# Kernel tuning notes

Hardware: AMD Instinct MI355X
Metric: run time of the kernel (lower is better)

## Reference

```python
import jax, jax.numpy as jnp
import numpy as np

B, X, H, R, M = 256, 512, 1024, 512, 512
F_BIAS = 1.0

def setup_inputs() -> dict:
    key = jax.random.key(0)
    ks = jax.random.split(key, 8)
    s = lambda fan: 1.0 / np.sqrt(fan)
    return {
        "x": jax.random.normal(ks[0], (B, X), jnp.float32),
        "h": jax.random.normal(ks[1], (B, H), jnp.float32),
        "c": jnp.tanh(jax.random.normal(ks[2], (B, H), jnp.float32)),
        "hmem": jax.random.normal(ks[3], (B, M, R), jnp.float32),
        "W_full": jax.random.normal(ks[4], (X + R + H, R + 4 * H), jnp.float32) * s(X + R + H),
        "bias": jnp.zeros((R + 4 * H,), jnp.float32),
        "W_full1": jax.random.normal(ks[5], (X + R + H, R + H), jnp.float32) * s(X + R + H),
        "bias1": jnp.zeros((R + H,), jnp.float32),
        "trans_w": jax.random.normal(ks[6], (R, X + H), jnp.float32) * s(X + H),
        "trans_b": jnp.zeros((R,), jnp.float32),
        "fc_w": jax.random.normal(ks[7], (M, X + H), jnp.float32) * s(X + H),
        "fc_b": jnp.zeros((M,), jnp.float32),
    }

def reference(x, h, c, hmem, W_full, bias, W_full1, bias1, trans_w, trans_b, fc_w, fc_b):
    h_size = H
    # soft read head over memory slots
    read_head = jnp.concatenate([x, c], axis=1) @ fc_w.T + fc_b          # [B, M]
    h_index = jax.nn.softmax(read_head, axis=1)                          # [B, M]
    h_entry = jnp.einsum('bm,bmr->br', h_index, hmem)                    # [B, R]
    # gated double-projection
    concat = jnp.concatenate([x, c, h_entry], axis=1)                    # [B, X+H+R]
    g = jax.nn.sigmoid(concat @ W_full1 + bias1)                         # [B, R+H]
    gate = jnp.concatenate([jnp.ones_like(x), g], axis=1)                # [B, X+H+R]
    pre = (concat * gate) @ W_full + bias                                # [B, R+4H]
    i = pre[:, 0*h_size:1*h_size]
    j = pre[:, 1*h_size:2*h_size]
    f = pre[:, 2*h_size:3*h_size]
    o = pre[:, 3*h_size:4*h_size]
    om = pre[:, 4*h_size:]                                               # [B, R]
    new_c = jnp.tanh(c * jax.nn.sigmoid(f + F_BIAS) + jax.nn.sigmoid(i) * jnp.tanh(j))
    new_h = new_c * jax.nn.sigmoid(o)
    r_out = h_entry * jax.nn.sigmoid(om)
    # steady-state write: soft index (detached), broadcast overwrite
    w_index = jax.lax.stop_gradient(h_index)                             # [B, M]
    w_val = jnp.concatenate([x, new_c], axis=1) @ trans_w.T + trans_b    # [B, R]
    new_hmem = w_val[:, None, :] * w_index[:, :, None] + hmem * (1.0 - w_index[:, :, None])
    new_r = jnp.concatenate([new_h, r_out], axis=1)                      # [B, H+R]
    return new_r, new_h, new_c, new_hmem
```

## Files before the change

### kernel.cpp

```cpp
#include <hip/hip_runtime.h>
#include <hip/hip_bf16.h>
#include <cstddef>

#define BB 256
#define XX 512
#define HH 1024
#define RR 512
#define MM 512
#define KCAT 2048
#define KXC 1536
#define NFULL 4608
#define NG 1536

#define OFF_NH (BB*1536)
#define OFF_NC (OFF_NH + BB*HH)
#define OFF_HM (OFF_NC + BB*HH)

#define WS_HIDX   0
#define WS_CONCAT (WS_HIDX + BB*MM)
#define WS_GATED  (WS_CONCAT + BB*KCAT)
#define WS_PRE    (WS_GATED + BB*KCAT)
#define WS_WVAL   (WS_PRE + BB*NFULL)

typedef __attribute__((ext_vector_type(8))) short bf16x8;
typedef __attribute__((ext_vector_type(4))) short s16x4;
typedef __attribute__((ext_vector_type(4))) float f32x4;

__device__ __forceinline__ float sigm(float x) { return 1.0f / (1.0f + expf(-x)); }

__device__ __forceinline__ unsigned short f2bf(float f) {
    unsigned u = __float_as_uint(f);
    u = u + 0x7fffu + ((u >> 16) & 1u);
    return (unsigned short)(u >> 16);
}
__device__ __forceinline__ float bf2f(unsigned short h) {
    return __uint_as_float((unsigned)h << 16);
}

__global__ __launch_bounds__(256) void prep_k(const float* __restrict__ x,
                                              const float* __restrict__ c,
                                              float* __restrict__ concatb,
                                              float* __restrict__ gated) {
    int idx = blockIdx.x * 256 + threadIdx.x;
    int b = idx / KXC, q = idx - b * KXC;
    float v;
    if (q < XX) {
        v = x[b * XX + q];
        gated[(size_t)b * KCAT + q] = v;
    } else {
        v = c[b * HH + (q - XX)];
    }
    concatb[(size_t)b * KCAT + q] = v;
}

template<int AMODE, int BLAYOUT, int EPI>
__global__ __launch_bounds__(256) void mgemm_k(const float* __restrict__ A0,
                                               const float* __restrict__ A1,
                                               const float* __restrict__ W,
                                               const float* __restrict__ bias,
                                               float* __restrict__ C,
                                               const float* __restrict__ E,
                                               int N, int K) {
    __shared__ __align__(16) short Ah[64][72];
    __shared__ __align__(16) short Al[64][72];
    __shared__ __align__(16) short Bh[64][72];
    __shared__ __align__(16) short Bl[64][72];

    const int tid = threadIdx.x;
    const int row0 = blockIdx.y * 64, col0 = blockIdx.x * 64;
    const int lane = tid & 63, w = tid >> 6;
    const int rm = (w >> 1) * 32, cn = (w & 1) * 32;
    const int fr = lane & 15;
    const int kg = lane >> 4;

    const int ar = tid >> 2;
    const int akq = (tid & 3) * 16;
    const int bkk = (tid >> 4) * 4;
    const int bnn = (tid & 15) * 4;

    f32x4 acc[2][2] = {};

    for (int k0 = 0; k0 < K; k0 += 64) {
        {
            const float* src;
            if (AMODE == 0) {
                src = A0 + (size_t)(row0 + ar) * K + k0 + akq;
            } else {
                int gk = k0 + akq;
                src = (gk < XX) ? (A0 + (size_t)(row0 + ar) * XX + gk)
                                : (A1 + (size_t)(row0 + ar) * HH + (gk - XX));
            }
            short hs[16], ls[16];
            #pragma unroll
            for (int q = 0; q < 4; ++q) {
                float4 v = reinterpret_cast<const float4*>(src)[q];
                float f[4] = {v.x, v.y, v.z, v.w};
                #pragma unroll
                for (int e = 0; e < 4; ++e) {
                    unsigned short hb = f2bf(f[e]);
                    hs[q * 4 + e] = (short)hb;
                    ls[q * 4 + e] = (short)f2bf(f[e] - bf2f(hb));
                }
            }
            *reinterpret_cast<bf16x8*>(&Ah[ar][akq])     = *reinterpret_cast<bf16x8*>(&hs[0]);
            *reinterpret_cast<bf16x8*>(&Ah[ar][akq + 8]) = *reinterpret_cast<bf16x8*>(&hs[8]);
            *reinterpret_cast<bf16x8*>(&Al[ar][akq])     = *reinterpret_cast<bf16x8*>(&ls[0]);
            *reinterpret_cast<bf16x8*>(&Al[ar][akq + 8]) = *reinterpret_cast<bf16x8*>(&ls[8]);
        }
        if (BLAYOUT == 1) {
            const float* src = W + (size_t)(col0 + ar) * K + k0 + akq;
            short hs[16], ls[16];
            #pragma unroll
            for (int q = 0; q < 4; ++q) {
                float4 v = reinterpret_cast<const float4*>(src)[q];
                float f[4] = {v.x, v.y, v.z, v.w};
                #pragma unroll
                for (int e = 0; e < 4; ++e) {
                    unsigned short hb = f2bf(f[e]);
                    hs[q * 4 + e] = (short)hb;
                    ls[q * 4 + e] = (short)f2bf(f[e] - bf2f(hb));
                }
            }
            *reinterpret_cast<bf16x8*>(&Bh[ar][akq])     = *reinterpret_cast<bf16x8*>(&hs[0]);
            *reinterpret_cast<bf16x8*>(&Bh[ar][akq + 8]) = *reinterpret_cast<bf16x8*>(&hs[8]);
            *reinterpret_cast<bf16x8*>(&Bl[ar][akq])     = *reinterpret_cast<bf16x8*>(&ls[0]);
            *reinterpret_cast<bf16x8*>(&Bl[ar][akq + 8]) = *reinterpret_cast<bf16x8*>(&ls[8]);
        } else {
            float4 r0 = *reinterpret_cast<const float4*>(W + (size_t)(k0 + bkk + 0) * N + col0 + bnn);
            float4 r1 = *reinterpret_cast<const float4*>(W + (size_t)(k0 + bkk + 1) * N + col0 + bnn);
            float4 r2 = *reinterpret_cast<const float4*>(W + (size_t)(k0 + bkk + 2) * N + col0 + bnn);
            float4 r3 = *reinterpret_cast<const float4*>(W + (size_t)(k0 + bkk + 3) * N + col0 + bnn);
            float col[4][4] = {{r0.x, r1.x, r2.x, r3.x},
                               {r0.y, r1.y, r2.y, r3.y},
                               {r0.z, r1.z, r2.z, r3.z},
                               {r0.w, r1.w, r2.w, r3.w}};
            #pragma unroll
            for (int j = 0; j < 4; ++j) {
                s16x4 hv, lv;
                #pragma unroll
                for (int e = 0; e < 4; ++e) {
                    unsigned short hb = f2bf(col[j][e]);
                    hv[e] = (short)hb;
                    lv[e] = (short)f2bf(col[j][e] - bf2f(hb));
                }
                *reinterpret_cast<s16x4*>(&Bh[bnn + j][bkk]) = hv;
                *reinterpret_cast<s16x4*>(&Bl[bnn + j][bkk]) = lv;
            }
        }
        __syncthreads();

        #pragma unroll
        for (int ks = 0; ks < 64; ks += 32) {
            bf16x8 ah[2], al[2], bh[2], bl[2];
            #pragma unroll
            for (int mf = 0; mf < 2; ++mf) {
                ah[mf] = *reinterpret_cast<const bf16x8*>(&Ah[rm + mf * 16 + fr][ks + kg * 8]);
                al[mf] = *reinterpret_cast<const bf16x8*>(&Al[rm + mf * 16 + fr][ks + kg * 8]);
            }
            #pragma unroll
            for (int nf = 0; nf < 2; ++nf) {
                bh[nf] = *reinterpret_cast<const bf16x8*>(&Bh[cn + nf * 16 + fr][ks + kg * 8]);
                bl[nf] = *reinterpret_cast<const bf16x8*>(&Bl[cn + nf * 16 + fr][ks + kg * 8]);
            }
            #pragma unroll
            for (int mf = 0; mf < 2; ++mf)
                #pragma unroll
                for (int nf = 0; nf < 2; ++nf) {
                    acc[mf][nf] = __builtin_amdgcn_mfma_f32_16x16x32_bf16(ah[mf], bh[nf], acc[mf][nf], 0, 0, 0);
                    acc[mf][nf] = __builtin_amdgcn_mfma_f32_16x16x32_bf16(ah[mf], bl[nf], acc[mf][nf], 0, 0, 0);
                    acc[mf][nf] = __builtin_amdgcn_mfma_f32_16x16x32_bf16(al[mf], bh[nf], acc[mf][nf], 0, 0, 0);
                }
        }
        __syncthreads();
    }

    #pragma unroll
    for (int mf = 0; mf < 2; ++mf)
        #pragma unroll
        for (int nf = 0; nf < 2; ++nf)
            #pragma unroll
            for (int i = 0; i < 4; ++i) {
                int row = row0 + rm + mf * 16 + kg * 4 + i;
                int col = col0 + cn + nf * 16 + fr;
                float v = acc[mf][nf][i] + bias[col];
                if (EPI == 0) {
                    C[(size_t)row * N + col] = v;
                } else {
                    size_t base = (size_t)row * KCAT + XX + col;
                    C[base] = E[base] * sigm(v);
                }
            }
}

__global__ __launch_bounds__(256) void softmax_k(float* __restrict__ rh) {
    int b = blockIdx.x;
    float* row = rh + (size_t)b * MM;
    int t = threadIdx.x;
    float v0 = row[t], v1 = row[t + 256];
    float m = fmaxf(v0, v1);
    #pragma unroll
    for (int off = 1; off < 64; off <<= 1) m = fmaxf(m, __shfl_xor(m, off));
    __shared__ float red[8];
    int wid = t >> 6, lane = t & 63;
    if (lane == 0) red[wid] = m;
    __syncthreads();
    float mm = fmaxf(fmaxf(red[0], red[1]), fmaxf(red[2], red[3]));
    float e0 = expf(v0 - mm), e1 = expf(v1 - mm);
    float s = e0 + e1;
    #pragma unroll
    for (int off = 1; off < 64; off <<= 1) s += __shfl_xor(s, off);
    if (lane == 0) red[4 + wid] = s;
    __syncthreads();
    float inv = 1.0f / (red[4] + red[5] + red[6] + red[7]);
    row[t] = e0 * inv;
    row[t + 256] = e1 * inv;
}

__global__ __launch_bounds__(512) void hentry_k(const float* __restrict__ hidx,
                                                const float* __restrict__ hmem,
                                                float* __restrict__ concatb) {
    int b = blockIdx.x;
    int r = threadIdx.x;
    __shared__ float wi[MM];
    wi[r] = hidx[(size_t)b * MM + r];
    __syncthreads();
    const float* hm = hmem + (size_t)b * MM * RR + r;
    float acc = 0.f;
    #pragma unroll 8
    for (int m = 0; m < MM; ++m) acc += wi[m] * hm[(size_t)m * RR];
    concatb[(size_t)b * KCAT + KXC + r] = acc;
}

__global__ __launch_bounds__(256) void lstm_k(const float* __restrict__ pre,
                                              const float* __restrict__ c,
                                              const float* __restrict__ concatb,
                                              float* __restrict__ out) {
    int idx = blockIdx.x * 256 + threadIdx.x;
    int b = idx / 1536, q = idx - b * 1536;
    const float* p = pre + (size_t)b * NFULL;
    if (q < HH) {
        float iv = p[q], jv = p[HH + q], fv = p[2 * HH + q], ov = p[3 * HH + q];
        float cc = c[(size_t)b * HH + q];
        float nc = tanhf(cc * sigm(fv + 1.0f) + sigm(iv) * tanhf(jv));
        float nh = nc * sigm(ov);
        out[(size_t)b * 1536 + q] = nh;
        out[OFF_NH + (size_t)b * HH + q] = nh;
        out[OFF_NC + (size_t)b * HH + q] = nc;
    } else {
        int r = q - HH;
        float om = p[4 * HH + r];
        float he = concatb[(size_t)b * KCAT + KXC + r];
        out[(size_t)b * 1536 + HH + r] = he * sigm(om);
    }
}

__global__ __launch_bounds__(256) void hmemupd_k(const float* __restrict__ hmem,
                                                 const float* __restrict__ wval,
                                                 const float* __restrict__ widx,
                                                 float* __restrict__ outhm) {
    size_t n4 = (size_t)BB * MM * RR / 4;
    size_t stride = (size_t)gridDim.x * blockDim.x;
    for (size_t i = (size_t)blockIdx.x * blockDim.x + threadIdx.x; i < n4; i += stride) {
        size_t e = i * 4;
        int r = (int)(e & (RR - 1));
        int m = (int)((e >> 9) & (MM - 1));
        int b = (int)(e >> 18);
        float wi = widx[(size_t)b * MM + m];
        float om = 1.0f - wi;
        float4 hv = *reinterpret_cast<const float4*>(hmem + e);
        float4 wv = *reinterpret_cast<const float4*>(wval + (size_t)b * RR + r);
        float4 o;
        o.x = wv.x * wi + hv.x * om;
        o.y = wv.y * wi + hv.y * om;
        o.z = wv.z * wi + hv.z * om;
        o.w = wv.w * wi + hv.w * om;
        *reinterpret_cast<float4*>(outhm + e) = o;
    }
}

extern "C" void kernel_launch(void* const* d_in, const int* in_sizes, int n_in,
                              void* d_out, int out_size, void* d_ws, size_t ws_size,
                              hipStream_t stream) {
    const float* x      = (const float*)d_in[0];
    const float* c      = (const float*)d_in[2];
    const float* hmem   = (const float*)d_in[3];
    const float* W_full = (const float*)d_in[4];
    const float* bias   = (const float*)d_in[5];
    const float* W_full1= (const float*)d_in[6];
    const float* bias1  = (const float*)d_in[7];
    const float* trans_w= (const float*)d_in[8];
    const float* trans_b= (const float*)d_in[9];
    const float* fc_w   = (const float*)d_in[10];
    const float* fc_b   = (const float*)d_in[11];

    float* out = (float*)d_out;
    float* ws  = (float*)d_ws;

    float* hidx    = ws + WS_HIDX;
    float* concatb = ws + WS_CONCAT;
    float* gated   = ws + WS_GATED;
    float* pre     = ws + WS_PRE;
    float* wval    = ws + WS_WVAL;
    float* new_c   = out + OFF_NC;

    prep_k<<<BB * KXC / 256, 256, 0, stream>>>(x, c, concatb, gated);

    mgemm_k<1, 1, 0><<<dim3(MM / 64, BB / 64), 256, 0, stream>>>(
        x, c, fc_w, fc_b, hidx, nullptr, MM, KXC);

    softmax_k<<<BB, 256, 0, stream>>>(hidx);

    hentry_k<<<BB, 512, 0, stream>>>(hidx, hmem, concatb);

    mgemm_k<0, 0, 1><<<dim3(NG / 64, BB / 64), 256, 0, stream>>>(
        concatb, nullptr, W_full1, bias1, gated, concatb, NG, KCAT);

    mgemm_k<0, 0, 0><<<dim3(NFULL / 64, BB / 64), 256, 0, stream>>>(
        gated, nullptr, W_full, bias, pre, nullptr, NFULL, KCAT);

    lstm_k<<<BB * 1536 / 256, 256, 0, stream>>>(pre, c, concatb, out);

    mgemm_k<1, 1, 0><<<dim3(RR / 64, BB / 64), 256, 0, stream>>>(
        x, new_c, trans_w, trans_b, wval, nullptr, RR, KXC);

    hmemupd_k<<<4096, 256, 0, stream>>>(hmem, wval, hidx, out + OFF_HM);
}
```

Before: 397.3 us.

## Pre-split weights and activations into bf16 hi/lo buffers before GEMMs

Adds kernels that convert each weight matrix once per call into transposed bf16 hi/lo pairs, and stores the activations (concat, gated, x/new_c) as hi/lo bf16 in workspace. The GEMM inner loop then only copies bf16 tiles instead of converting fp32 in every block. Softmax and the h_entry reduction are fused into one kernel. The cost is extra conversion launches and memory traffic for the weights on every call, plus a larger workspace, with a fallback to the old path when the workspace is too small.

```diff
diff --git a/kernel.cpp b/kernel.cpp
--- a/kernel.cpp
+++ b/kernel.cpp
@@ -16,12 +16,6 @@
 #define OFF_NC (OFF_NH + BB*HH)
 #define OFF_HM (OFF_NC + BB*HH)
 
-#define WS_HIDX   0
-#define WS_CONCAT (WS_HIDX + BB*MM)
-#define WS_GATED  (WS_CONCAT + BB*KCAT)
-#define WS_PRE    (WS_GATED + BB*KCAT)
-#define WS_WVAL   (WS_PRE + BB*NFULL)
-
 typedef __attribute__((ext_vector_type(8))) short bf16x8;
 typedef __attribute__((ext_vector_type(4))) short s16x4;
 typedef __attribute__((ext_vector_type(4))) float f32x4;
@@ -37,30 +31,105 @@
     return __uint_as_float((unsigned)h << 16);
 }
 
+
+__global__ __launch_bounds__(256) void convw_k(const float* __restrict__ src,
+                                               short* __restrict__ hi,
+                                               short* __restrict__ lo,
+                                               int n8) {
+    int i = blockIdx.x * 256 + threadIdx.x;
+    if (i >= n8) return;
+    size_t e0 = (size_t)i * 8;
+    short hs[8], ls[8];
+    #pragma unroll
+    for (int q = 0; q < 2; ++q) {
+        float4 v = reinterpret_cast<const float4*>(src + e0)[q];
+        float f[4] = {v.x, v.y, v.z, v.w};
+        #pragma unroll
+        for (int e = 0; e < 4; ++e) {
+            unsigned short hb = f2bf(f[e]);
+            hs[q * 4 + e] = (short)hb;
+            ls[q * 4 + e] = (short)f2bf(f[e] - bf2f(hb));
+        }
+    }
+    *reinterpret_cast<bf16x8*>(hi + e0) = *reinterpret_cast<bf16x8*>(&hs[0]);
+    *reinterpret_cast<bf16x8*>(lo + e0) = *reinterpret_cast<bf16x8*>(&ls[0]);
+}
+
+__global__ __launch_bounds__(256) void convt_k(const float* __restrict__ W,
+                                               int Kdim, int Ndim,
+                                               short* __restrict__ Thi,
+                                               short* __restrict__ Tlo) {
+    __shared__ __align__(16) short lh[64][72];
+    __shared__ __align__(16) short ll[64][72];
+    const int tid = threadIdx.x;
+    const int k0 = blockIdx.x * 64, n0 = blockIdx.y * 64;
+    {
+        int kr = (tid >> 4) * 4;
+        int nc = (tid & 15) * 4;
+        #pragma unroll
+        for (int i = 0; i < 4; ++i) {
+            float4 v = *reinterpret_cast<const float4*>(W + (size_t)(k0 + kr + i) * Ndim + n0 + nc);
+            float f[4] = {v.x, v.y, v.z, v.w};
+            #pragma unroll
+            for (int e = 0; e < 4; ++e) {
+                unsigned short hb = f2bf(f[e]);
+                lh[nc + e][kr + i] = (short)hb;
+                ll[nc + e][kr + i] = (short)f2bf(f[e] - bf2f(hb));
+            }
+        }
+    }
+    __syncthreads();
+    {
+        int nl = tid >> 2;
+        int kq = (tid & 3) * 16;
+        size_t base = (size_t)(n0 + nl) * Kdim + k0 + kq;
+        *reinterpret_cast<bf16x8*>(Thi + base)     = *reinterpret_cast<const bf16x8*>(&lh[nl][kq]);
+        *reinterpret_cast<bf16x8*>(Thi + base + 8) = *reinterpret_cast<const bf16x8*>(&lh[nl][kq + 8]);
+        *reinterpret_cast<bf16x8*>(Tlo + base)     = *reinterpret_cast<const bf16x8*>(&ll[nl][kq]);
+        *reinterpret_cast<bf16x8*>(Tlo + base + 8) = *reinterpret_cast<const bf16x8*>(&ll[nl][kq + 8]);
+    }
+}
+
 __global__ __launch_bounds__(256) void prep_k(const float* __restrict__ x,
                                               const float* __restrict__ c,
-                                              float* __restrict__ concatb,
-                                              float* __restrict__ gated) {
-    int idx = blockIdx.x * 256 + threadIdx.x;
-    int b = idx / KXC, q = idx - b * KXC;
-    float v;
+                                              short* __restrict__ cat_hi, short* __restrict__ cat_lo,
+                                              short* __restrict__ gat_hi, short* __restrict__ gat_lo,
+                                              short* __restrict__ xnc_hi, short* __restrict__ xnc_lo) {
+    int i = blockIdx.x * 256 + threadIdx.x;
+    int e0 = i * 4;
+    int b = e0 / KXC, q = e0 - b * KXC;
+    float4 v = (q < XX) ? *reinterpret_cast<const float4*>(x + (size_t)b * XX + q)
+                        : *reinterpret_cast<const float4*>(c + (size_t)b * HH + (q - XX));
+    float f[4] = {v.x, v.y, v.z, v.w};
+    s16x4 hv, lv;
+    #pragma unroll
+    for (int e = 0; e < 4; ++e) {
+        unsigned short hb = f2bf(f[e]);
+        hv[e] = (short)hb;
+        lv[e] = (short)f2bf(f[e] - bf2f(hb));
+    }
+    *reinterpret_cast<s16x4*>(cat_hi + (size_t)b * KCAT + q) = hv;
+    *reinterpret_cast<s16x4*>(cat_lo + (size_t)b * KCAT + q) = lv;
     if (q < XX) {
-        v = x[b * XX + q];
-        gated[(size_t)b * KCAT + q] = v;
-    } else {
-        v = c[b * HH + (q - XX)];
-    }
-    concatb[(size_t)b * KCAT + q] = v;
-}
-
-template<int AMODE, int BLAYOUT, int EPI>
-__global__ __launch_bounds__(256) void mgemm_k(const float* __restrict__ A0,
-                                               const float* __restrict__ A1,
-                                               const float* __restrict__ W,
-                                               const float* __restrict__ bias,
-                                               float* __restrict__ C,
-                                               const float* __restrict__ E,
-                                               int N, int K) {
+        *reinterpret_cast<s16x4*>(gat_hi + (size_t)b * KCAT + q) = hv;
+        *reinterpret_cast<s16x4*>(gat_lo + (size_t)b * KCAT + q) = lv;
+        *reinterpret_cast<s16x4*>(xnc_hi + (size_t)b * KXC + q) = hv;
+        *reinterpret_cast<s16x4*>(xnc_lo + (size_t)b * KXC + q) = lv;
+    }
+}
+
+template<int EPI>
+__global__ __launch_bounds__(256) void mgemm_ps(const short* __restrict__ Ahi,
+                                                const short* __restrict__ Alo, int lda,
+                                                const short* __restrict__ Bhi,
+                                                const short* __restrict__ Blo,
+                                                const float* __restrict__ bias,
+                                                float* __restrict__ C, int ldc,
+                                                const short* __restrict__ cat_hi,
+                                                const short* __restrict__ cat_lo,
+                                                short* __restrict__ gat_hi,
+                                                short* __restrict__ gat_lo,
+                                                int K) {
     __shared__ __align__(16) short Ah[64][72];
     __shared__ __align__(16) short Al[64][72];
     __shared__ __align__(16) short Bh[64][72];
@@ -75,77 +144,31 @@
 
     const int ar = tid >> 2;
     const int akq = (tid & 3) * 16;
-    const int bkk = (tid >> 4) * 4;
-    const int bnn = (tid & 15) * 4;
 
     f32x4 acc[2][2] = {};
 
     for (int k0 = 0; k0 < K; k0 += 64) {
         {
-            const float* src;
-            if (AMODE == 0) {
-                src = A0 + (size_t)(row0 + ar) * K + k0 + akq;
-            } else {
-                int gk = k0 + akq;
-                src = (gk < XX) ? (A0 + (size_t)(row0 + ar) * XX + gk)
-                                : (A1 + (size_t)(row0 + ar) * HH + (gk - XX));
-            }
-            short hs[16], ls[16];
-            #pragma unroll
-            for (int q = 0; q < 4; ++q) {
-                float4 v = reinterpret_cast<const float4*>(src)[q];
-                float f[4] = {v.x, v.y, v.z, v.w};
-                #pragma unroll
-                for (int e = 0; e < 4; ++e) {
-                    unsigned short hb = f2bf(f[e]);
-                    hs[q * 4 + e] = (short)hb;
-                    ls[q * 4 + e] = (short)f2bf(f[e] - bf2f(hb));
-                }
-            }
-            *reinterpret_cast<bf16x8*>(&Ah[ar][akq])     = *reinterpret_cast<bf16x8*>(&hs[0]);
-            *reinterpret_cast<bf16x8*>(&Ah[ar][akq + 8]) = *reinterpret_cast<bf16x8*>(&hs[8]);
-            *reinterpret_cast<bf16x8*>(&Al[ar][akq])     = *reinterpret_cast<bf16x8*>(&ls[0]);
-            *reinterpret_cast<bf16x8*>(&Al[ar][akq + 8]) = *reinterpret_cast<bf16x8*>(&ls[8]);
-        }
-        if (BLAYOUT == 1) {
-            const float* src = W + (size_t)(col0 + ar) * K + k0 + akq;
-            short hs[16], ls[16];
-            #pragma unroll
-            for (int q = 0; q < 4; ++q) {
-                float4 v = reinterpret_cast<const float4*>(src)[q];
-                float f[4] = {v.x, v.y, v.z, v.w};
-                #pragma unroll
-                for (int e = 0; e < 4; ++e) {
-                    unsigned short hb = f2bf(f[e]);
-                    hs[q * 4 + e] = (short)hb;
-                    ls[q * 4 + e] = (short)f2bf(f[e] - bf2f(hb));
-                }
-            }
-            *reinterpret_cast<bf16x8*>(&Bh[ar][akq])     = *reinterpret_cast<bf16x8*>(&hs[0]);
-            *reinterpret_cast<bf16x8*>(&Bh[ar][akq + 8]) = *reinterpret_cast<bf16x8*>(&hs[8]);
-            *reinterpret_cast<bf16x8*>(&Bl[ar][akq])     = *reinterpret_cast<bf16x8*>(&ls[0]);
-            *reinterpret_cast<bf16x8*>(&Bl[ar][akq + 8]) = *reinterpret_cast<bf16x8*>(&ls[8]);
-        } else {
-            float4 r0 = *reinterpret_cast<const float4*>(W + (size_t)(k0 + bkk + 0) * N + col0 + bnn);
-            float4 r1 = *reinterpret_cast<const float4*>(W + (size_t)(k0 + bkk + 1) * N + col0 + bnn);
-            float4 r2 = *reinterpret_cast<const float4*>(W + (size_t)(k0 + bkk + 2) * N + col0 + bnn);
-            float4 r3 = *reinterpret_cast<const float4*>(W + (size_t)(k0 + bkk + 3) * N + col0 + bnn);
-            float col[4][4] = {{r0.x, r1.x, r2.x, r3.x},
-                               {r0.y, r1.y, r2.y, r3.y},
-                               {r0.z, r1.z, r2.z, r3.z},
-                               {r0.w, r1.w, r2.w, r3.w}};
-            #pragma unroll
-            for (int j = 0; j < 4; ++j) {
-                s16x4 hv, lv;
-                #pragma unroll
-                for (int e = 0; e < 4; ++e) {
-                    unsigned short hb = f2bf(col[j][e]);
-                    hv[e] = (short)hb;
-                    lv[e] = (short)f2bf(col[j][e] - bf2f(hb));
-                }
-                *reinterpret_cast<s16x4*>(&Bh[bnn + j][bkk]) = hv;
-                *reinterpret_cast<s16x4*>(&Bl[bnn + j][bkk]) = lv;
-            }
+            size_t base = (size_t)(row0 + ar) * lda + k0 + akq;
+            bf16x8 h0 = *reinterpret_cast<const bf16x8*>(Ahi + base);
+            bf16x8 h1 = *reinterpret_cast<const bf16x8*>(Ahi + base + 8);
+            bf16x8 l0 = *reinterpret_cast<const bf16x8*>(Alo + base);
+            bf16x8 l1 = *reinterpret_cast<const bf16x8*>(Alo + base + 8);
+            *reinterpret_cast<bf16x8*>(&Ah[ar][akq])     = h0;
+            *reinterpret_cast<bf16x8*>(&Ah[ar][akq + 8]) = h1;
+            *reinterpret_cast<bf16x8*>(&Al[ar][akq])     = l0;
+            *reinterpret_cast<bf16x8*>(&Al[ar][akq + 8]) = l1;
+        }
+        {
+            size_t base = (size_t)(col0 + ar) * K + k0 + akq;
+            bf16x8 h0 = *reinterpret_cast<const bf16x8*>(Bhi + base);
+            bf16x8 h1 = *reinterpret_cast<const bf16x8*>(Bhi + base + 8);
+            bf16x8 l0 = *reinterpret_cast<const bf16x8*>(Blo + base);
+            bf16x8 l1 = *reinterpret_cast<const bf16x8*>(Blo + base + 8);
+            *reinterpret_cast<bf16x8*>(&Bh[ar][akq])     = h0;
+            *reinterpret_cast<bf16x8*>(&Bh[ar][akq + 8]) = h1;
+            *reinterpret_cast<bf16x8*>(&Bl[ar][akq])     = l0;
+            *reinterpret_cast<bf16x8*>(&Bl[ar][akq + 8]) = l1;
         }
         __syncthreads();
 
@@ -184,57 +207,67 @@
                 int col = col0 + cn + nf * 16 + fr;
                 float v = acc[mf][nf][i] + bias[col];
                 if (EPI == 0) {
-                    C[(size_t)row * N + col] = v;
+                    C[(size_t)row * ldc + col] = v;
                 } else {
                     size_t base = (size_t)row * KCAT + XX + col;
-                    C[base] = E[base] * sigm(v);
+                    float e = bf2f((unsigned short)cat_hi[base]) + bf2f((unsigned short)cat_lo[base]);
+                    float gv = e * sigm(v);
+                    unsigned short hb = f2bf(gv);
+                    gat_hi[base] = (short)hb;
+                    gat_lo[base] = (short)f2bf(gv - bf2f(hb));
                 }
             }
 }
 
-__global__ __launch_bounds__(256) void softmax_k(float* __restrict__ rh) {
-    int b = blockIdx.x;
-    float* row = rh + (size_t)b * MM;
-    int t = threadIdx.x;
-    float v0 = row[t], v1 = row[t + 256];
-    float m = fmaxf(v0, v1);
+__global__ __launch_bounds__(512) void smhe_k(const float* __restrict__ rh,
+                                              const float* __restrict__ hmem,
+                                              float* __restrict__ hidx,
+                                              short* __restrict__ cat_hi,
+                                              short* __restrict__ cat_lo) {
+    __shared__ float red[8];
+    __shared__ float red2[8];
+    __shared__ float wiL[MM];
+    int b = blockIdx.x, t = threadIdx.x;
+    float v = rh[(size_t)b * MM + t];
+    float m = v;
     #pragma unroll
     for (int off = 1; off < 64; off <<= 1) m = fmaxf(m, __shfl_xor(m, off));
-    __shared__ float red[8];
     int wid = t >> 6, lane = t & 63;
     if (lane == 0) red[wid] = m;
     __syncthreads();
-    float mm = fmaxf(fmaxf(red[0], red[1]), fmaxf(red[2], red[3]));
-    float e0 = expf(v0 - mm), e1 = expf(v1 - mm);
-    float s = e0 + e1;
+    float mm = red[0];
+    #pragma unroll
+    for (int i = 1; i < 8; ++i) mm = fmaxf(mm, red[i]);
+    float e = expf(v - mm);
+    float s = e;
     #pragma unroll
     for (int off = 1; off < 64; off <<= 1) s += __shfl_xor(s, off);
-    if (lane == 0) red[4 + wid] = s;
+    if (lane == 0) red2[wid] = s;
     __syncthreads();
-    float inv = 1.0f / (red[4] + red[5] + red[6] + red[7]);
-    row[t] = e0 * inv;
-    row[t + 256] = e1 * inv;
-}
-
-__global__ __launch_bounds__(512) void hentry_k(const float* __restrict__ hidx,
-                                                const float* __restrict__ hmem,
-                                                float* __restrict__ concatb) {
-    int b = blockIdx.x;
-    int r = threadIdx.x;
-    __shared__ float wi[MM];
-    wi[r] = hidx[(size_t)b * MM + r];
+    float tot = red2[0];
+    #pragma unroll
+    for (int i = 1; i < 8; ++i) tot += red2[i];
+    float wi = e / tot;
+    hidx[(size_t)b * MM + t] = wi;
+    wiL[t] = wi;
     __syncthreads();
-    const float* hm = hmem + (size_t)b * MM * RR + r;
+    const float* hm = hmem + (size_t)b * MM * RR + t;
     float acc = 0.f;
     #pragma unroll 8
-    for (int m = 0; m < MM; ++m) acc += wi[m] * hm[(size_t)m * RR];
-    concatb[(size_t)b * KCAT + KXC + r] = acc;
+    for (int m2 = 0; m2 < MM; ++m2) acc += wiL[m2] * hm[(size_t)m2 * RR];
+    size_t base = (size_t)b * KCAT + KXC + t;
+    unsigned short hb = f2bf(acc);
+    cat_hi[base] = (short)hb;
+    cat_lo[base] = (short)f2bf(acc - bf2f(hb));
 }
 
 __global__ __launch_bounds__(256) void lstm_k(const float* __restrict__ pre,
                                               const float* __restrict__ c,
-                                              const float* __restrict__ concatb,
-                                              float* __restrict__ out) {
+                                              const short* __restrict__ cat_hi,
+                                              const short* __restrict__ cat_lo,
+                                              float* __restrict__ out,
+                                              short* __restrict__ xnc_hi,
+                                              short* __restrict__ xnc_lo) {
     int idx = blockIdx.x * 256 + threadIdx.x;
     int b = idx / 1536, q = idx - b * 1536;
     const float* p = pre + (size_t)b * NFULL;
@@ -246,10 +279,14 @@
         out[(size_t)b * 1536 + q] = nh;
         out[OFF_NH + (size_t)b * HH + q] = nh;
         out[OFF_NC + (size_t)b * HH + q] = nc;
+        unsigned short hb = f2bf(nc);
+        xnc_hi[(size_t)b * KXC + XX + q] = (short)hb;
+        xnc_lo[(size_t)b * KXC + XX + q] = (short)f2bf(nc - bf2f(hb));
     } else {
         int r = q - HH;
         float om = p[4 * HH + r];
-        float he = concatb[(size_t)b * KCAT + KXC + r];
+        size_t base = (size_t)b * KCAT + KXC + r;
+        float he = bf2f((unsigned short)cat_hi[base]) + bf2f((unsigned short)cat_lo[base]);
         out[(size_t)b * 1536 + HH + r] = he * sigm(om);
     }
 }
@@ -278,6 +315,207 @@
     }
 }
 
+
+__global__ __launch_bounds__(256) void prep3_k(const float* __restrict__ x,
+                                               const float* __restrict__ c,
+                                               float* __restrict__ concatb,
+                                               float* __restrict__ gated) {
+    int idx = blockIdx.x * 256 + threadIdx.x;
+    int b = idx / KXC, q = idx - b * KXC;
+    float v;
+    if (q < XX) { v = x[b * XX + q]; gated[(size_t)b * KCAT + q] = v; }
+    else v = c[b * HH + (q - XX)];
+    concatb[(size_t)b * KCAT + q] = v;
+}
+
+template<int AMODE, int BLAYOUT, int EPI>
+__global__ __launch_bounds__(256) void mgemm3_k(const float* __restrict__ A0,
+                                                const float* __restrict__ A1,
+                                                const float* __restrict__ W,
+                                                const float* __restrict__ bias,
+                                                float* __restrict__ C,
+                                                const float* __restrict__ E,
+                                                int N, int K) {
+    __shared__ __align__(16) short Ah[64][72];
+    __shared__ __align__(16) short Al[64][72];
+    __shared__ __align__(16) short Bh[64][72];
+    __shared__ __align__(16) short Bl[64][72];
+    const int tid = threadIdx.x;
+    const int row0 = blockIdx.y * 64, col0 = blockIdx.x * 64;
+    const int lane = tid & 63, w = tid >> 6;
+    const int rm = (w >> 1) * 32, cn = (w & 1) * 32;
+    const int fr = lane & 15, kg = lane >> 4;
+    const int ar = tid >> 2, akq = (tid & 3) * 16;
+    const int bkk = (tid >> 4) * 4, bnn = (tid & 15) * 4;
+    f32x4 acc[2][2] = {};
+    for (int k0 = 0; k0 < K; k0 += 64) {
+        {
+            const float* src;
+            if (AMODE == 0) src = A0 + (size_t)(row0 + ar) * K + k0 + akq;
+            else {
+                int gk = k0 + akq;
+                src = (gk < XX) ? (A0 + (size_t)(row0 + ar) * XX + gk)
+                                : (A1 + (size_t)(row0 + ar) * HH + (gk - XX));
+            }
+            short hs[16], ls[16];
+            #pragma unroll
+            for (int q = 0; q < 4; ++q) {
+                float4 v = reinterpret_cast<const float4*>(src)[q];
+                float f[4] = {v.x, v.y, v.z, v.w};
+                #pragma unroll
+                for (int e = 0; e < 4; ++e) {
+                    unsigned short hb = f2bf(f[e]);
+                    hs[q * 4 + e] = (short)hb;
+                    ls[q * 4 + e] = (short)f2bf(f[e] - bf2f(hb));
+                }
+            }
+            *reinterpret_cast<bf16x8*>(&Ah[ar][akq])     = *reinterpret_cast<bf16x8*>(&hs[0]);
+            *reinterpret_cast<bf16x8*>(&Ah[ar][akq + 8]) = *reinterpret_cast<bf16x8*>(&hs[8]);
+            *reinterpret_cast<bf16x8*>(&Al[ar][akq])     = *reinterpret_cast<bf16x8*>(&ls[0]);
+            *reinterpret_cast<bf16x8*>(&Al[ar][akq + 8]) = *reinterpret_cast<bf16x8*>(&ls[8]);
+        }
+        if (BLAYOUT == 1) {
+            const float* src = W + (size_t)(col0 + ar) * K + k0 + akq;
+            short hs[16], ls[16];
+            #pragma unroll
+            for (int q = 0; q < 4; ++q) {
+                float4 v = reinterpret_cast<const float4*>(src)[q];
+                float f[4] = {v.x, v.y, v.z, v.w};
+                #pragma unroll
+                for (int e = 0; e < 4; ++e) {
+                    unsigned short hb = f2bf(f[e]);
+                    hs[q * 4 + e] = (short)hb;
+                    ls[q * 4 + e] = (short)f2bf(f[e] - bf2f(hb));
+                }
+            }
+            *reinterpret_cast<bf16x8*>(&Bh[ar][akq])     = *reinterpret_cast<bf16x8*>(&hs[0]);
+            *reinterpret_cast<bf16x8*>(&Bh[ar][akq + 8]) = *reinterpret_cast<bf16x8*>(&hs[8]);
+            *reinterpret_cast<bf16x8*>(&Bl[ar][akq])     = *reinterpret_cast<bf16x8*>(&ls[0]);
+            *reinterpret_cast<bf16x8*>(&Bl[ar][akq + 8]) = *reinterpret_cast<bf16x8*>(&ls[8]);
+        } else {
+            float4 r0 = *reinterpret_cast<const float4*>(W + (size_t)(k0 + bkk + 0) * N + col0 + bnn);
+            float4 r1 = *reinterpret_cast<const float4*>(W + (size_t)(k0 + bkk + 1) * N + col0 + bnn);
+            float4 r2 = *reinterpret_cast<const float4*>(W + (size_t)(k0 + bkk + 2) * N + col0 + bnn);
+            float4 r3 = *reinterpret_cast<const float4*>(W + (size_t)(k0 + bkk + 3) * N + col0 + bnn);
+            float col[4][4] = {{r0.x, r1.x, r2.x, r3.x}, {r0.y, r1.y, r2.y, r3.y},
+                               {r0.z, r1.z, r2.z, r3.z}, {r0.w, r1.w, r2.w, r3.w}};
+            #pragma unroll
+            for (int j = 0; j < 4; ++j) {
+                s16x4 hv, lv;
+                #pragma unroll
+                for (int e = 0; e < 4; ++e) {
+                    unsigned short hb = f2bf(col[j][e]);
+                    hv[e] = (short)hb;
+                    lv[e] = (short)f2bf(col[j][e] - bf2f(hb));
+                }
+                *reinterpret_cast<s16x4*>(&Bh[bnn + j][bkk]) = hv;
+                *reinterpret_cast<s16x4*>(&Bl[bnn + j][bkk]) = lv;
+            }
+        }
+        __syncthreads();
+        #pragma unroll
+        for (int ks = 0; ks < 64; ks += 32) {
+            bf16x8 ah[2], al[2], bh[2], bl[2];
+            #pragma unroll
+            for (int mf = 0; mf < 2; ++mf) {
+                ah[mf] = *reinterpret_cast<const bf16x8*>(&Ah[rm + mf * 16 + fr][ks + kg * 8]);
+                al[mf] = *reinterpret_cast<const bf16x8*>(&Al[rm + mf * 16 + fr][ks + kg * 8]);
+            }
+            #pragma unroll
+            for (int nf = 0; nf < 2; ++nf) {
+                bh[nf] = *reinterpret_cast<const bf16x8*>(&Bh[cn + nf * 16 + fr][ks + kg * 8]);
+                bl[nf] = *reinterpret_cast<const bf16x8*>(&Bl[cn + nf * 16 + fr][ks + kg * 8]);
+            }
+            #pragma unroll
+            for (int mf = 0; mf < 2; ++mf)
+                #pragma unroll
+                for (int nf = 0; nf < 2; ++nf) {
+                    acc[mf][nf] = __builtin_amdgcn_mfma_f32_16x16x32_bf16(ah[mf], bh[nf], acc[mf][nf], 0, 0, 0);
+                    acc[mf][nf] = __builtin_amdgcn_mfma_f32_16x16x32_bf16(ah[mf], bl[nf], acc[mf][nf], 0, 0, 0);
+                    acc[mf][nf] = __builtin_amdgcn_mfma_f32_16x16x32_bf16(al[mf], bh[nf], acc[mf][nf], 0, 0, 0);
+                }
+        }
+        __syncthreads();
+    }
+    #pragma unroll
+    for (int mf = 0; mf < 2; ++mf)
+        #pragma unroll
+        for (int nf = 0; nf < 2; ++nf)
+            #pragma unroll
+            for (int i = 0; i < 4; ++i) {
+                int row = row0 + rm + mf * 16 + kg * 4 + i;
+                int col = col0 + cn + nf * 16 + fr;
+                float v = acc[mf][nf][i] + bias[col];
+                if (EPI == 0) C[(size_t)row * N + col] = v;
+                else {
+                    size_t base = (size_t)row * KCAT + XX + col;
+                    C[base] = E[base] * sigm(v);
+                }
+            }
+}
+
+__global__ __launch_bounds__(256) void softmax3_k(float* __restrict__ rh) {
+    int b = blockIdx.x;
+    float* row = rh + (size_t)b * MM;
+    int t = threadIdx.x;
+    float v0 = row[t], v1 = row[t + 256];
+    float m = fmaxf(v0, v1);
+    #pragma unroll
+    for (int off = 1; off < 64; off <<= 1) m = fmaxf(m, __shfl_xor(m, off));
+    __shared__ float red[8];
+    int wid = t >> 6, lane = t & 63;
+    if (lane == 0) red[wid] = m;
+    __syncthreads();
+    float mm = fmaxf(fmaxf(red[0], red[1]), fmaxf(red[2], red[3]));
+    float e0 = expf(v0 - mm), e1 = expf(v1 - mm);
+    float s = e0 + e1;
+    #pragma unroll
+    for (int off = 1; off < 64; off <<= 1) s += __shfl_xor(s, off);
+    if (lane == 0) red[4 + wid] = s;
+    __syncthreads();
+    float inv = 1.0f / (red[4] + red[5] + red[6] + red[7]);
+    row[t] = e0 * inv;
+    row[t + 256] = e1 * inv;
+}
+
+__global__ __launch_bounds__(512) void hentry3_k(const float* __restrict__ hidx,
+                                                 const float* __restrict__ hmem,
+                                                 float* __restrict__ concatb) {
+    int b = blockIdx.x;
+    int r = threadIdx.x;
+    __shared__ float wi[MM];
+    wi[r] = hidx[(size_t)b * MM + r];
+    __syncthreads();
+    const float* hm = hmem + (size_t)b * MM * RR + r;
+    float acc = 0.f;
+    #pragma unroll 8
+    for (int m = 0; m < MM; ++m) acc += wi[m] * hm[(size_t)m * RR];
+    concatb[(size_t)b * KCAT + KXC + r] = acc;
+}
+
+__global__ __launch_bounds__(256) void lstm3_k(const float* __restrict__ pre,
+                                               const float* __restrict__ c,
+                                               const float* __restrict__ concatb,
+                                               float* __restrict__ out) {
+    int idx = blockIdx.x * 256 + threadIdx.x;
+    int b = idx / 1536, q = idx - b * 1536;
+    const float* p = pre + (size_t)b * NFULL;
+    if (q < HH) {
+        float iv = p[q], jv = p[HH + q], fv = p[2 * HH + q], ov = p[3 * HH + q];
+        float cc = c[(size_t)b * HH + q];
+        float nc = tanhf(cc * sigm(fv + 1.0f) + sigm(iv) * tanhf(jv));
+        float nh = nc * sigm(ov);
+        out[(size_t)b * 1536 + q] = nh;
+        out[OFF_NH + (size_t)b * HH + q] = nh;
+        out[OFF_NC + (size_t)b * HH + q] = nc;
+    } else {
+        int r = q - HH;
+        float om = p[4 * HH + r];
+        float he = concatb[(size_t)b * KCAT + KXC + r];
+        out[(size_t)b * 1536 + HH + r] = he * sigm(om);
+    }
+}
+
 extern "C" void kernel_launch(void* const* d_in, const int* in_sizes, int n_in,
                               void* d_out, int out_size, void* d_ws, size_t ws_size,
                               hipStream_t stream) {
@@ -294,34 +532,88 @@
     const float* fc_b   = (const float*)d_in[11];
 
     float* out = (float*)d_out;
-    float* ws  = (float*)d_ws;
-
-    float* hidx    = ws + WS_HIDX;
-    float* concatb = ws + WS_CONCAT;
-    float* gated   = ws + WS_GATED;
-    float* pre     = ws + WS_PRE;
-    float* wval    = ws + WS_WVAL;
-    float* new_c   = out + OFF_NC;
-
-    prep_k<<<BB * KXC / 256, 256, 0, stream>>>(x, c, concatb, gated);
-
-    mgemm_k<1, 1, 0><<<dim3(MM / 64, BB / 64), 256, 0, stream>>>(
-        x, c, fc_w, fc_b, hidx, nullptr, MM, KXC);
-
-    softmax_k<<<BB, 256, 0, stream>>>(hidx);
-
-    hentry_k<<<BB, 512, 0, stream>>>(hidx, hmem, concatb);
-
-    mgemm_k<0, 0, 1><<<dim3(NG / 64, BB / 64), 256, 0, stream>>>(
-        concatb, nullptr, W_full1, bias1, gated, concatb, NG, KCAT);
-
-    mgemm_k<0, 0, 0><<<dim3(NFULL / 64, BB / 64), 256, 0, stream>>>(
-        gated, nullptr, W_full, bias, pre, nullptr, NFULL, KCAT);
-
-    lstm_k<<<BB * 1536 / 256, 256, 0, stream>>>(pre, c, concatb, out);
-
-    mgemm_k<1, 1, 0><<<dim3(RR / 64, BB / 64), 256, 0, stream>>>(
-        x, new_c, trans_w, trans_b, wval, nullptr, RR, KXC);
-
-    hmemupd_k<<<4096, 256, 0, stream>>>(hmem, wval, hidx, out + OFF_HM);
-}
+
+    constexpr size_t SZ_WT  = (size_t)NFULL * KCAT * 2;
+    constexpr size_t SZ_WT1 = (size_t)NG * KCAT * 2;
+    constexpr size_t SZ_FCW = (size_t)MM * KXC * 2;
+    constexpr size_t SZ_TRW = (size_t)RR * KXC * 2;
+    constexpr size_t SZ_CAT = (size_t)BB * KCAT * 2;
+    constexpr size_t SZ_XNC = (size_t)BB * KXC * 2;
+    constexpr size_t SZ_RH  = (size_t)BB * MM * 4;
+    constexpr size_t SZ_PRE = (size_t)BB * NFULL * 4;
+    constexpr size_t NEED = 2*SZ_WT + 2*SZ_WT1 + 2*SZ_FCW + 2*SZ_TRW
+                          + 4*SZ_CAT + 2*SZ_XNC + 2*SZ_RH + SZ_PRE + SZ_RH;
+
+    if (ws_size >= NEED) {
+        char* p = (char*)d_ws;
+        short* wt_hi  = (short*)p; p += SZ_WT;
+        short* wt_lo  = (short*)p; p += SZ_WT;
+        short* wt1_hi = (short*)p; p += SZ_WT1;
+        short* wt1_lo = (short*)p; p += SZ_WT1;
+        short* fcw_hi = (short*)p; p += SZ_FCW;
+        short* fcw_lo = (short*)p; p += SZ_FCW;
+        short* trw_hi = (short*)p; p += SZ_TRW;
+        short* trw_lo = (short*)p; p += SZ_TRW;
+        short* cat_hi = (short*)p; p += SZ_CAT;
+        short* cat_lo = (short*)p; p += SZ_CAT;
+        short* gat_hi = (short*)p; p += SZ_CAT;
+        short* gat_lo = (short*)p; p += SZ_CAT;
+        short* xnc_hi = (short*)p; p += SZ_XNC;
+        short* xnc_lo = (short*)p; p += SZ_XNC;
+        float* rh     = (float*)p; p += SZ_RH;
+        float* hidx   = (float*)p; p += SZ_RH;
+        float* pre    = (float*)p; p += SZ_PRE;
+        float* wval   = (float*)p;
+
+        convt_k<<<dim3(KCAT / 64, NFULL / 64), 256, 0, stream>>>(W_full, KCAT, NFULL, wt_hi, wt_lo);
+        convt_k<<<dim3(KCAT / 64, NG / 64), 256, 0, stream>>>(W_full1, KCAT, NG, wt1_hi, wt1_lo);
+        convw_k<<<(MM * KXC / 8 + 255) / 256, 256, 0, stream>>>(fc_w, fcw_hi, fcw_lo, MM * KXC / 8);
+        convw_k<<<(RR * KXC / 8 + 255) / 256, 256, 0, stream>>>(trans_w, trw_hi, trw_lo, RR * KXC / 8);
+
+        prep_k<<<BB * KXC / 4 / 256, 256, 0, stream>>>(x, c, cat_hi, cat_lo, gat_hi, gat_lo, xnc_hi, xnc_lo);
+
+        mgemm_ps<0><<<dim3(MM / 64, BB / 64), 256, 0, stream>>>(
+            cat_hi, cat_lo, KCAT, fcw_hi, fcw_lo, fc_b, rh, MM,
+            nullptr, nullptr, nullptr, nullptr, KXC);
+
+        smhe_k<<<BB, 512, 0, stream>>>(rh, hmem, hidx, cat_hi, cat_lo);
+
+        mgemm_ps<1><<<dim3(NG / 64, BB / 64), 256, 0, stream>>>(
+            cat_hi, cat_lo, KCAT, wt1_hi, wt1_lo, bias1, nullptr, 0,
+            cat_hi, cat_lo, gat_hi, gat_lo, KCAT);
+
+        mgemm_ps<0><<<dim3(NFULL / 64, BB / 64), 256, 0, stream>>>(
+            gat_hi, gat_lo, KCAT, wt_hi, wt_lo, bias, pre, NFULL,
+            nullptr, nullptr, nullptr, nullptr, KCAT);
+
+        lstm_k<<<BB * 1536 / 256, 256, 0, stream>>>(pre, c, cat_hi, cat_lo, out, xnc_hi, xnc_lo);
+
+        mgemm_ps<0><<<dim3(RR / 64, BB / 64), 256, 0, stream>>>(
+            xnc_hi, xnc_lo, KXC, trw_hi, trw_lo, trans_b, wval, RR,
+            nullptr, nullptr, nullptr, nullptr, KXC);
+
+        hmemupd_k<<<4096, 256, 0, stream>>>(hmem, wval, hidx, out + OFF_HM);
+    } else {
+        float* ws   = (float*)d_ws;
+        float* hidx    = ws;
+        float* concatb = hidx + BB * MM;
+        float* gated   = concatb + BB * KCAT;
+        float* pre     = gated + BB * KCAT;
+        float* wval    = pre + BB * NFULL;
+        float* new_c   = out + OFF_NC;
+
+        prep3_k<<<BB * KXC / 256, 256, 0, stream>>>(x, c, concatb, gated);
+        mgemm3_k<1, 1, 0><<<dim3(MM / 64, BB / 64), 256, 0, stream>>>(
+            x, c, fc_w, fc_b, hidx, nullptr, MM, KXC);
+        softmax3_k<<<BB, 256, 0, stream>>>(hidx);
+        hentry3_k<<<BB, 512, 0, stream>>>(hidx, hmem, concatb);
+        mgemm3_k<0, 0, 1><<<dim3(NG / 64, BB / 64), 256, 0, stream>>>(
+            concatb, nullptr, W_full1, bias1, gated, concatb, NG, KCAT);
+        mgemm3_k<0, 0, 0><<<dim3(NFULL / 64, BB / 64), 256, 0, stream>>>(
+            gated, nullptr, W_full, bias, pre, nullptr, NFULL, KCAT);
+        lstm3_k<<<BB * 1536 / 256, 256, 0, stream>>>(pre, c, concatb, out);
+        mgemm3_k<1, 1, 0><<<dim3(RR / 64, BB / 64), 256, 0, stream>>>(
+            x, new_c, trans_w, trans_b, wval, nullptr, RR, KXC);
+        hmemupd_k<<<4096, 256, 0, stream>>>(hmem, wval, hidx, out + OFF_HM);
+    }
+}
```

Measured after the change: 341.7 us, median of 4. 1.16x faster.
